# Kernel tuning notes

Measured on AMD Instinct MI355X. Metric: run time of the kernel, lower is better.

## Reference

```python
import jax, jax.numpy as jnp
import numpy as np

IN_CH = 512
OUT_CH = 512
NUM_GROUPS = 32
EPS = 1e-5


def setup_inputs() -> dict:
    key = jax.random.key(0)
    ks = jax.random.split(key, 8)
    N, C, H, W = 4, IN_CH, 64, 64
    s = 0.02
    return {
        "x": jax.random.normal(ks[0], (N, C, H, W), jnp.float32),
        "gn_scale": jnp.ones((C,), jnp.float32),
        "gn_bias": jnp.zeros((C,), jnp.float32),
        "wq": jax.random.normal(ks[1], (OUT_CH, C), jnp.float32) * s,
        "bq": jnp.zeros((OUT_CH,), jnp.float32),
        "wk": jax.random.normal(ks[2], (OUT_CH, C), jnp.float32) * s,
        "bk": jnp.zeros((OUT_CH,), jnp.float32),
        "wv": jax.random.normal(ks[3], (OUT_CH, C), jnp.float32) * s,
        "bv": jnp.zeros((OUT_CH,), jnp.float32),
        "wo": jax.random.normal(ks[4], (OUT_CH, OUT_CH), jnp.float32) * s,
        "bo": jnp.zeros((OUT_CH,), jnp.float32),
    }


def _group_norm(x, scale, bias):
    # x: [N, C, H, W] -> normalize per (group, spatial)
    N, C, H, W = x.shape
    g = x.reshape(N, NUM_GROUPS, C // NUM_GROUPS, H, W)
    mean = jnp.mean(g, axis=(2, 3, 4), keepdims=True)
    var = jnp.var(g, axis=(2, 3, 4), keepdims=True)
    g = (g - mean) * jax.lax.rsqrt(var + EPS)
    h = g.reshape(N, C, H, W)
    return h * scale[None, :, None, None] + bias[None, :, None, None]


def _conv1x1(x, w, b):
    # x: [N, C_in, H, W], w: [C_out, C_in] -> [N, C_out, H, W]
    return jnp.einsum('nchw,dc->ndhw', x, w) + b[None, :, None, None]


def reference(x, gn_scale, gn_bias, wq, bq, wk, bk, wv, bv, wo, bo):
    N, C, H, W = x.shape
    L = H * W
    h = _group_norm(x, gn_scale, gn_bias)
    q = _conv1x1(h, wq, bq).reshape(N, OUT_CH, L)
    k = _conv1x1(h, wk, bk).reshape(N, OUT_CH, L)
    v = _conv1x1(h, wv, bv).reshape(N, OUT_CH, L)
    scores = jnp.einsum('nci,ncj->nij', q, k) * (OUT_CH ** -0.5)  # [N, L, L]
    att = jax.nn.softmax(scores, axis=-1)
    out = jnp.einsum('nij,ncj->nci', att, v).reshape(N, OUT_CH, H, W)
    out = _conv1x1(out, wo, bo)
    return out + x  # skip_proj is Identity since in_ch == out_ch
```

## Files before the change

kernel.cpp:

```cpp
#include <hip/hip_runtime.h>
#include <math.h>

#define NB   4
#define CCH  512
#define LL   4096
#define GRP  32
#define CPG  16
#define CL   (CCH*LL)
#define EPSV 1e-5f
#define QSTR 1024

typedef __bf16 bf16x8 __attribute__((ext_vector_type(8)));
typedef float  f32x4  __attribute__((ext_vector_type(4)));

#define GLOAD_LDS16(g, l) __builtin_amdgcn_global_load_lds( \
    (const __attribute__((address_space(1))) void*)(g),     \
    (__attribute__((address_space(3))) void*)(l), 16, 0, 0)

__device__ __forceinline__ int swz_slot(int row, int q) {
    return 4 * row + (q ^ ((row >> 1) & 3));
}
__device__ __forceinline__ void swz_src(int l, int& jj, int& cc) {
    jj = l >> 2;
    cc = (l & 3) ^ ((l >> 3) & 3);
}

#define DPPF(x, ctrl) __builtin_bit_cast(float, \
    __builtin_amdgcn_update_dpp(0, __builtin_bit_cast(int, (x)), (ctrl), 0xf, 0xf, false))
__device__ __forceinline__ float red_sum16(float x) {
    x += DPPF(x, 0xB1); x += DPPF(x, 0x4E);
    x += DPPF(x, 0x124); x += DPPF(x, 0x128);
    return x;
}

__global__ __launch_bounds__(1024) void gn_stats(const float* __restrict__ x,
                                                 float* __restrict__ stats) {
    int n = blockIdx.x >> 5, g = blockIdx.x & 31;
    size_t base = ((size_t)n * CCH + (size_t)g * CPG) * LL;
    const float4* xp = (const float4*)(x + base);
    const int NV = CPG * LL / 4;
    int tid = threadIdx.x;
    float s1 = 0.f, s2 = 0.f;
    for (int i = tid; i < NV; i += 1024) {
        float4 v = xp[i];
        s1 += v.x + v.y + v.z + v.w;
        s2 += v.x*v.x + v.y*v.y + v.z*v.z + v.w*v.w;
    }
    __shared__ float red[32];
    for (int o = 32; o; o >>= 1) { s1 += __shfl_down(s1, o); s2 += __shfl_down(s2, o); }
    int lane = tid & 63, w = tid >> 6;
    if (!lane) { red[w] = s1; red[16 + w] = s2; }
    __syncthreads();
    if (tid == 0) {
        float a = 0.f, b = 0.f;
        for (int i = 0; i < 16; ++i) { a += red[i]; b += red[16 + i]; }
        const float inv_n = 1.f / (float)(CPG * LL);
        float mean = a * inv_n;
        float var  = b * inv_n - mean * mean;
        stats[blockIdx.x * 2]     = mean;
        stats[blockIdx.x * 2 + 1] = rsqrtf(var + EPSV);
    }
}

__global__ __launch_bounds__(256) void gn_norm_t(const float* __restrict__ x,
    const float* __restrict__ gamma, const float* __restrict__ beta,
    const float* __restrict__ stats, __bf16* __restrict__ Ht) {
    __shared__ float T[64][65];
    int n = blockIdx.z, c0 = blockIdx.y * 64, l0 = blockIdx.x * 64;
    int tid = threadIdx.x;
    int lx = tid & 63, py = tid >> 6;
    const float* xb = x + (size_t)n * CL;
#pragma unroll
    for (int p = 0; p < 16; ++p) {
        int cl = p * 4 + py;
        int c = c0 + cl;
        int g = c >> 4;
        float mean = stats[(n * GRP + g) * 2];
        float rstd = stats[(n * GRP + g) * 2 + 1];
        float sc = gamma[c] * rstd, bi = beta[c] - mean * sc;
        float v = xb[(size_t)c * LL + l0 + lx];
        T[lx][cl] = v * sc + bi;
    }
    __syncthreads();
    __bf16* hb = Ht + (size_t)n * CL;
#pragma unroll
    for (int p = 0; p < 16; ++p) {
        int ll = p * 4 + py;
        hb[(size_t)(l0 + ll) * CCH + c0 + lx] = (__bf16)T[ll][lx];
    }
}

__global__ __launch_bounds__(256) void tobf16_4(
    const float* __restrict__ s0, const float* __restrict__ s1,
    const float* __restrict__ s2, const float* __restrict__ s3,
    __bf16* __restrict__ dst) {
    const float* sp = (blockIdx.y == 0) ? s0 : (blockIdx.y == 1) ? s1
                    : (blockIdx.y == 2) ? s2 : s3;
    int i = (blockIdx.x * 256 + threadIdx.x) * 4;
    float4 v = *(const float4*)(sp + i);
    __bf16* d = dst + (size_t)blockIdx.y * CCH * CCH + i;
    d[0] = (__bf16)v.x; d[1] = (__bf16)v.y; d[2] = (__bf16)v.z; d[3] = (__bf16)v.w;
}

#define BM 128
#define BN 128
#define BK 32

template<int EPI>
__global__ __launch_bounds__(256) void gemm_nt(
    const __bf16* __restrict__ A, const __bf16* __restrict__ B,
    void* __restrict__ Cv, int M, int N, int K,
    long bsA, long bsB, long bsC, long bsR,
    const float* __restrict__ bias, const float* __restrict__ bias2,
    const float* __restrict__ resid)
{
    __shared__ __align__(16) __bf16 As[BM * BK];
    __shared__ __align__(16) __bf16 Bs[BN * BK];
    const int tid = threadIdx.x;
    const int l = tid & 63, w = tid >> 6;
    const int wm = w >> 1, wn = w & 1;
    const int m0 = blockIdx.y * BM, n0 = blockIdx.x * BN;
    A += (long)blockIdx.z * bsA;
    B += (long)blockIdx.z * bsB;

    f32x4 acc[4][4];
#pragma unroll
    for (int i = 0; i < 4; ++i)
#pragma unroll
        for (int j = 0; j < 4; ++j) acc[i][j] = f32x4{0.f, 0.f, 0.f, 0.f};

    int jj, cc; swz_src(l, jj, cc);
    const int slot = swz_slot(l & 15, l >> 4);

    const __bf16* Ag = A + (size_t)(m0 + w * 16 + jj) * K + cc * 8;
    const __bf16* Bg = B + (size_t)(n0 + w * 16 + jj) * K + cc * 8;
    char* AsB = (char*)As + w * 1024;
    char* BsB = (char*)Bs + w * 1024;

    for (int k0 = 0; k0 < K; k0 += BK) {
        GLOAD_LDS16(Ag + k0,                 AsB);
        GLOAD_LDS16(Ag + k0 + (size_t)64*K,  AsB + 4096);
        GLOAD_LDS16(Bg + k0,                 BsB);
        GLOAD_LDS16(Bg + k0 + (size_t)64*K,  BsB + 4096);
        __syncthreads();
        bf16x8 ar[4], br[4];
#pragma unroll
        for (int t = 0; t < 4; ++t) {
            ar[t] = *(const bf16x8*)(As + (wm*64 + t*16) * BK + slot * 8);
            br[t] = *(const bf16x8*)(Bs + (wn*64 + t*16) * BK + slot * 8);
        }
#pragma unroll
        for (int ti = 0; ti < 4; ++ti)
#pragma unroll
            for (int tj = 0; tj < 4; ++tj)
                acc[ti][tj] = __builtin_amdgcn_mfma_f32_16x16x32_bf16(
                    ar[ti], br[tj], acc[ti][tj], 0, 0, 0);
        __syncthreads();
    }

    const long cb = (long)blockIdx.z * bsC;
    const float* bn = (EPI == 5) ? ((n0 < 512) ? bias : (bias2 - 512)) : nullptr;
#pragma unroll
    for (int ti = 0; ti < 4; ++ti) {
#pragma unroll
        for (int r = 0; r < 4; ++r) {
            int m = m0 + wm*64 + ti*16 + (l >> 4)*4 + r;
            float bv = (EPI == 2 || EPI == 4) ? bias[m] : 0.f;
#pragma unroll
            for (int tj = 0; tj < 4; ++tj) {
                int n = n0 + wn*64 + tj*16 + (l & 15);
                float v = acc[ti][tj][r];
                if (EPI == 5) v += bn[n];
                if (EPI == 2 || EPI == 4) v += bv;
                if (EPI == 4) {
                    float rs = resid[(long)blockIdx.z * bsR + (size_t)m * N + n];
                    ((float*)Cv)[cb + (size_t)m * N + n] = v + rs;
                } else {
                    ((__bf16*)Cv)[cb + (size_t)m * N + n] = (__bf16)v;
                }
            }
        }
    }
}

#define PSTR 88

__global__ __launch_bounds__(512, 2) void flash_attn(
    const __bf16* __restrict__ QK, const __bf16* __restrict__ Vb,
    __bf16* __restrict__ Ot)
{
    __shared__ __align__(16) __bf16 Ks[16 * 64 * 32];
    __shared__ __align__(16) __bf16 Vs[2 * 512 * 32];
    __shared__ float  Sm[64 * 68];
    __shared__ __align__(16) __bf16 Ps[64 * PSTR];
    __shared__ float Lp[64 * 2];

    const int tid = threadIdx.x;
    const int l = tid & 63, w = tid >> 6;
    const int wi = w & 1, jh = (w >> 1) & 1, kh = w >> 2;
    const int g = l >> 4, c = l & 15;
    const int b = (blockIdx.x & 7) >> 1;
    const int qt = ((blockIdx.x >> 3) << 1) | (blockIdx.x & 1);
    const int i0 = qt * 64;
    const size_t bb2 = (size_t)b * LL * QSTR;
    const size_t bb  = (size_t)b * CL;
    const float alpha = 0.044194173824159216f;

    int jj, cc; swz_src(l, jj, cc);
    const int slot = swz_slot(c, g);

    bf16x8 Qf[2][8];
    {
        const __bf16* Qg = QK + bb2 + (size_t)(i0 + wi*32 + c) * QSTR + kh*256 + g*8;
#pragma unroll
        for (int mi = 0; mi < 2; ++mi)
#pragma unroll
            for (int kc = 0; kc < 8; ++kc)
                Qf[mi][kc] = *(const bf16x8*)(Qg + (size_t)mi*16*QSTR + kc*32);
    }

    f32x4 Oacc[4][4];
#pragma unroll
    for (int mi = 0; mi < 4; ++mi)
#pragma unroll
        for (int ni = 0; ni < 4; ++ni) Oacc[mi][ni] = f32x4{0.f, 0.f, 0.f, 0.f};
    float l_r[2][4] = {{0.f,0.f,0.f,0.f},{0.f,0.f,0.f,0.f}};

    const __bf16* Kb = QK + bb2 + 512;
    const __bf16* Vg = Vb + bb;

    auto stageK = [&](int j0) {
#pragma unroll
        for (int q = 0; q < 2; ++q) {
            int kc = q * 8 + w;
#pragma unroll
            for (int p = 0; p < 4; ++p) {
                const __bf16* src = Kb + (size_t)(j0 + p*16 + jj) * QSTR + kc*32 + cc*8;
                GLOAD_LDS16(src, (char*)Ks + kc*4096 + p*1024);
            }
        }
    };
    auto stageV = [&](int j0) {
#pragma unroll
        for (int jc = 0; jc < 2; ++jc)
#pragma unroll
            for (int p = 0; p < 4; ++p) {
                const __bf16* src = Vg + (size_t)(w*64 + p*16 + jj) * LL + j0 + jc*32 + cc*8;
                GLOAD_LDS16(src, (char*)Vs + jc*32768 + (w*64 + p*16)*64);
            }
    };

    stageK(0);
    for (int t = 0; t < 64; ++t) {
        __syncthreads();
        stageV(t * 64);

        f32x4 S[2][2];
#pragma unroll
        for (int mi = 0; mi < 2; ++mi)
#pragma unroll
            for (int tj = 0; tj < 2; ++tj) S[mi][tj] = f32x4{0.f,0.f,0.f,0.f};
#pragma unroll
        for (int kc = 0; kc < 8; ++kc) {
#pragma unroll
            for (int tj = 0; tj < 2; ++tj) {
                bf16x8 kf = *(const bf16x8*)(Ks + (kh*8 + kc)*2048 + (jh*2 + tj)*512 + slot*8);
#pragma unroll
                for (int mi = 0; mi < 2; ++mi)
                    S[mi][tj] = __builtin_amdgcn_mfma_f32_16x16x32_bf16(Qf[mi][kc], kf, S[mi][tj], 0, 0, 0);
            }
        }
        if (kh) {
#pragma unroll
            for (int mi = 0; mi < 2; ++mi)
#pragma unroll
                for (int tj = 0; tj < 2; ++tj)
#pragma unroll
                    for (int r = 0; r < 4; ++r)
                        Sm[(wi*32 + mi*16 + g*4 + r)*68 + (jh*2 + tj)*16 + c] = S[mi][tj][r];
        }
        __syncthreads();

        if (!kh) {
#pragma unroll
            for (int mi = 0; mi < 2; ++mi) {
#pragma unroll
                for (int r = 0; r < 4; ++r) {
                    int row = wi*32 + mi*16 + g*4 + r;
                    float rs = 0.f;
#pragma unroll
                    for (int tj = 0; tj < 2; ++tj) {
                        float p = __expf((S[mi][tj][r] + Sm[row*68 + (jh*2 + tj)*16 + c]) * alpha);
                        rs += p;
                        Ps[row * PSTR + (jh*2 + tj)*16 + c] = (__bf16)p;
                    }
                    l_r[mi][r] += rs;
                }
            }
        } else {
            if (t < 63) stageK((t + 1) * 64);
        }
        __syncthreads();
        if (t < 63 && !kh) stageK((t + 1) * 64);

#pragma unroll
        for (int jc = 0; jc < 2; ++jc) {
            bf16x8 pa[4];
#pragma unroll
            for (int mi = 0; mi < 4; ++mi)
                pa[mi] = *(const bf16x8*)(Ps + (mi*16 + c) * PSTR + jc*32 + g*8);
#pragma unroll
            for (int ni = 0; ni < 4; ++ni) {
                bf16x8 vf = *(const bf16x8*)(Vs + jc*16384 + (w*64 + ni*16)*32 + slot*8);
#pragma unroll
                for (int mi = 0; mi < 4; ++mi)
                    Oacc[mi][ni] = __builtin_amdgcn_mfma_f32_16x16x32_bf16(pa[mi], vf, Oacc[mi][ni], 0, 0, 0);
            }
        }
    }

    if (!kh) {
#pragma unroll
        for (int mi = 0; mi < 2; ++mi)
#pragma unroll
            for (int r = 0; r < 4; ++r) {
                float tot = red_sum16(l_r[mi][r]);
                if (c == 0) Lp[(wi*32 + mi*16 + g*4 + r)*2 + jh] = tot;
            }
    }
    __syncthreads();
#pragma unroll
    for (int mi = 0; mi < 4; ++mi) {
#pragma unroll
        for (int r = 0; r < 4; ++r) {
            int row = mi*16 + g*4 + r;
            float inv = 1.f / (Lp[row*2] + Lp[row*2 + 1]);
#pragma unroll
            for (int ni = 0; ni < 4; ++ni) {
                int col = w*64 + ni*16 + c;
                Ot[bb + (size_t)(i0 + row) * CCH + col] = (__bf16)(Oacc[mi][ni][r] * inv);
            }
        }
    }
}

extern "C" void kernel_launch(void* const* d_in, const int* in_sizes, int n_in,
                              void* d_out, int out_size, void* d_ws, size_t ws_size,
                              hipStream_t stream) {
    const float* x   = (const float*)d_in[0];
    const float* gnw = (const float*)d_in[1];
    const float* gnb = (const float*)d_in[2];
    const float* wq  = (const float*)d_in[3];
    const float* bq  = (const float*)d_in[4];
    const float* wk  = (const float*)d_in[5];
    const float* bk  = (const float*)d_in[6];
    const float* wv  = (const float*)d_in[7];
    const float* bv  = (const float*)d_in[8];
    const float* wo  = (const float*)d_in[9];
    const float* bo  = (const float*)d_in[10];
    float* out = (float*)d_out;

    __bf16* wsb = (__bf16*)d_ws;
    const size_t NCL = (size_t)NB * CL;
    __bf16* Ht  = wsb;
    __bf16* QKt = Ht + NCL;
    __bf16* Vb  = QKt + 2 * NCL;
    __bf16* Ot  = Vb + NCL;
    __bf16* Wb  = Ot + NCL;
    float* stats = (float*)(Wb + (size_t)4 * CCH * CCH);
    __bf16* wqkb = Wb;
    __bf16* wvb  = Wb + (size_t)2 * CCH * CCH;
    __bf16* wob  = Wb + (size_t)3 * CCH * CCH;

    tobf16_4<<<dim3(256, 4), 256, 0, stream>>>(wq, wk, wv, wo, Wb);
    gn_stats<<<NB * GRP, 1024, 0, stream>>>(x, stats);
    gn_norm_t<<<dim3(LL / 64, CCH / 64, NB), 256, 0, stream>>>(x, gnw, gnb, stats, Ht);

    gemm_nt<5><<<dim3(1024 / 128, LL / 128, NB), 256, 0, stream>>>(
        Ht, wqkb, QKt, LL, 1024, CCH, CL, 0, (long)LL * 1024, 0, bq, bk, nullptr);
    gemm_nt<2><<<dim3(LL / 128, CCH / 128, NB), 256, 0, stream>>>(
        wvb, Ht, Vb, CCH, LL, CCH, 0, CL, CL, 0, bv, nullptr, nullptr);

    flash_attn<<<dim3(256), 512, 0, stream>>>(QKt, Vb, Ot);

    gemm_nt<4><<<dim3(LL / 128, CCH / 128, NB), 256, 0, stream>>>(
        wob, Ot, (void*)out, CCH, LL, CCH, 0, CL, CL, CL, bo, nullptr, x);
}
```

Before: 388.9 us.

## Double-buffer K tiles, load V directly to registers, split softmax across halves

The flash attention loop now keeps K in two LDS buffers, so the next tile is staged while the current one is consumed, and the extra barrier for K staging is gone. V fragments are read straight from global memory into registers instead of being staged through LDS. The softmax work is split so both kh halves exchange partial scores via a transposed Sm layout and each computes exp for 16 rows, balancing work. The cost is higher register pressure from holding V fragments and uncoalesced direct global V loads.

```diff
diff --git a/kernel.cpp b/kernel.cpp
--- a/kernel.cpp
+++ b/kernel.cpp
@@ -184,14 +184,15 @@
 }
 
 #define PSTR 88
+#define SMSTR 68
 
 __global__ __launch_bounds__(512, 2) void flash_attn(
     const __bf16* __restrict__ QK, const __bf16* __restrict__ Vb,
     __bf16* __restrict__ Ot)
 {
-    __shared__ __align__(16) __bf16 Ks[16 * 64 * 32];
-    __shared__ __align__(16) __bf16 Vs[2 * 512 * 32];
-    __shared__ float  Sm[64 * 68];
+    __shared__ __align__(16) __bf16 Ks0[16 * 64 * 32];
+    __shared__ __align__(16) __bf16 Ks1[16 * 64 * 32];
+    __shared__ __align__(16) float  Sm[64 * SMSTR];
     __shared__ __align__(16) __bf16 Ps[64 * PSTR];
     __shared__ float Lp[64 * 2];
 
@@ -224,109 +225,111 @@
     for (int mi = 0; mi < 4; ++mi)
 #pragma unroll
         for (int ni = 0; ni < 4; ++ni) Oacc[mi][ni] = f32x4{0.f, 0.f, 0.f, 0.f};
-    float l_r[2][4] = {{0.f,0.f,0.f,0.f},{0.f,0.f,0.f,0.f}};
+    float l_r[4] = {0.f, 0.f, 0.f, 0.f};
 
     const __bf16* Kb = QK + bb2 + 512;
     const __bf16* Vg = Vb + bb;
 
-    auto stageK = [&](int j0) {
+    auto stageK = [&](__bf16* dst, int j0) {
 #pragma unroll
         for (int q = 0; q < 2; ++q) {
             int kc = q * 8 + w;
 #pragma unroll
             for (int p = 0; p < 4; ++p) {
                 const __bf16* src = Kb + (size_t)(j0 + p*16 + jj) * QSTR + kc*32 + cc*8;
-                GLOAD_LDS16(src, (char*)Ks + kc*4096 + p*1024);
+                GLOAD_LDS16(src, (char*)dst + kc*4096 + p*1024);
             }
         }
     };
-    auto stageV = [&](int j0) {
-#pragma unroll
-        for (int jc = 0; jc < 2; ++jc)
-#pragma unroll
-            for (int p = 0; p < 4; ++p) {
-                const __bf16* src = Vg + (size_t)(w*64 + p*16 + jj) * LL + j0 + jc*32 + cc*8;
-                GLOAD_LDS16(src, (char*)Vs + jc*32768 + (w*64 + p*16)*64);
-            }
-    };
-
-    stageK(0);
-    for (int t = 0; t < 64; ++t) {
-        __syncthreads();
-        stageV(t * 64);
-
-        f32x4 S[2][2];
-#pragma unroll
-        for (int mi = 0; mi < 2; ++mi)
-#pragma unroll
-            for (int tj = 0; tj < 2; ++tj) S[mi][tj] = f32x4{0.f,0.f,0.f,0.f};
-#pragma unroll
-        for (int kc = 0; kc < 8; ++kc) {
-#pragma unroll
-            for (int tj = 0; tj < 2; ++tj) {
-                bf16x8 kf = *(const bf16x8*)(Ks + (kh*8 + kc)*2048 + (jh*2 + tj)*512 + slot*8);
-#pragma unroll
-                for (int mi = 0; mi < 2; ++mi)
-                    S[mi][tj] = __builtin_amdgcn_mfma_f32_16x16x32_bf16(Qf[mi][kc], kf, S[mi][tj], 0, 0, 0);
-            }
-        }
-        if (kh) {
+
+    stageK(Ks0, 0);
+    __syncthreads();
+
+    for (int tt = 0; tt < 32; ++tt) {
+#pragma unroll
+        for (int h = 0; h < 2; ++h) {
+            const int t = tt * 2 + h;
+            __bf16* const Krd = h ? Ks1 : Ks0;
+            __bf16* const Kst = h ? Ks0 : Ks1;
+
+            bf16x8 vf[2][4];
+            const __bf16* Vt = Vg + t * 64;
+#pragma unroll
+            for (int jc = 0; jc < 2; ++jc)
+#pragma unroll
+                for (int ni = 0; ni < 4; ++ni)
+                    vf[jc][ni] = *(const bf16x8*)(
+                        Vt + (size_t)(w*64 + ni*16 + c) * LL + jc*32 + g*8);
+
+            if (t < 63) stageK(Kst, (t + 1) * 64);
+
+            f32x4 S[2][2];
 #pragma unroll
             for (int mi = 0; mi < 2; ++mi)
 #pragma unroll
+                for (int tj = 0; tj < 2; ++tj) S[mi][tj] = f32x4{0.f,0.f,0.f,0.f};
+#pragma unroll
+            for (int kc = 0; kc < 8; ++kc) {
+#pragma unroll
+                for (int tj = 0; tj < 2; ++tj) {
+                    bf16x8 kf = *(const bf16x8*)(
+                        Krd + (kh*8 + kc)*2048 + (jh*2 + tj)*512 + slot*8);
+#pragma unroll
+                    for (int mi = 0; mi < 2; ++mi)
+                        S[mi][tj] = __builtin_amdgcn_mfma_f32_16x16x32_bf16(
+                            Qf[mi][kc], kf, S[mi][tj], 0, 0, 0);
+                }
+            }
+            {
+                const int me = 1 - kh;
+#pragma unroll
                 for (int tj = 0; tj < 2; ++tj)
-#pragma unroll
-                    for (int r = 0; r < 4; ++r)
-                        Sm[(wi*32 + mi*16 + g*4 + r)*68 + (jh*2 + tj)*16 + c] = S[mi][tj][r];
-        }
-        __syncthreads();
-
-        if (!kh) {
-#pragma unroll
-            for (int mi = 0; mi < 2; ++mi) {
+                    *(f32x4*)&Sm[(jh*32 + tj*16 + c) * SMSTR + wi*32 + me*16 + g*4]
+                        = S[me][tj];
+            }
+            __syncthreads();
+
+            {
+                f32x4 part[2];
+#pragma unroll
+                for (int tj = 0; tj < 2; ++tj)
+                    part[tj] = *(const f32x4*)&Sm[(jh*32 + tj*16 + c) * SMSTR
+                                                  + wi*32 + kh*16 + g*4];
+                const int row0 = wi*32 + kh*16 + g*4;
 #pragma unroll
                 for (int r = 0; r < 4; ++r) {
-                    int row = wi*32 + mi*16 + g*4 + r;
                     float rs = 0.f;
 #pragma unroll
                     for (int tj = 0; tj < 2; ++tj) {
-                        float p = __expf((S[mi][tj][r] + Sm[row*68 + (jh*2 + tj)*16 + c]) * alpha);
+                        float p = __expf((S[kh][tj][r] + part[tj][r]) * alpha);
                         rs += p;
-                        Ps[row * PSTR + (jh*2 + tj)*16 + c] = (__bf16)p;
+                        Ps[(row0 + r) * PSTR + jh*32 + tj*16 + c] = (__bf16)p;
                     }
-                    l_r[mi][r] += rs;
+                    l_r[r] += rs;
                 }
             }
-        } else {
-            if (t < 63) stageK((t + 1) * 64);
-        }
-        __syncthreads();
-        if (t < 63 && !kh) stageK((t + 1) * 64);
-
-#pragma unroll
-        for (int jc = 0; jc < 2; ++jc) {
-            bf16x8 pa[4];
-#pragma unroll
-            for (int mi = 0; mi < 4; ++mi)
-                pa[mi] = *(const bf16x8*)(Ps + (mi*16 + c) * PSTR + jc*32 + g*8);
-#pragma unroll
-            for (int ni = 0; ni < 4; ++ni) {
-                bf16x8 vf = *(const bf16x8*)(Vs + jc*16384 + (w*64 + ni*16)*32 + slot*8);
+            __syncthreads();
+
+#pragma unroll
+            for (int jc = 0; jc < 2; ++jc) {
+                bf16x8 pa[4];
 #pragma unroll
                 for (int mi = 0; mi < 4; ++mi)
-                    Oacc[mi][ni] = __builtin_amdgcn_mfma_f32_16x16x32_bf16(pa[mi], vf, Oacc[mi][ni], 0, 0, 0);
-            }
-        }
-    }
-
-    if (!kh) {
-#pragma unroll
-        for (int mi = 0; mi < 2; ++mi)
-#pragma unroll
-            for (int r = 0; r < 4; ++r) {
-                float tot = red_sum16(l_r[mi][r]);
-                if (c == 0) Lp[(wi*32 + mi*16 + g*4 + r)*2 + jh] = tot;
-            }
+                    pa[mi] = *(const bf16x8*)(Ps + (mi*16 + c) * PSTR + jc*32 + g*8);
+#pragma unroll
+                for (int ni = 0; ni < 4; ++ni)
+#pragma unroll
+                    for (int mi = 0; mi < 4; ++mi)
+                        Oacc[mi][ni] = __builtin_amdgcn_mfma_f32_16x16x32_bf16(
+                            pa[mi], vf[jc][ni], Oacc[mi][ni], 0, 0, 0);
+            }
+        }
+    }
+
+#pragma unroll
+    for (int r = 0; r < 4; ++r) {
+        float tot = red_sum16(l_r[r]);
+        if (c == 0) Lp[(wi*32 + kh*16 + g*4 + r)*2 + jh] = tot;
     }
     __syncthreads();
 #pragma unroll
```

Result: slower. 525.3 us (+35.1%).

## Split softmax exp work across both K-half waves and add MFMA priority hints

Applied to the files above, without the earlier changes.

Before, the waves owning the second K half only wrote partial scores, and the first-half waves did all the exp and P writes. Now each wave sends the partial for the other half's rows and computes exp for its own 16 rows, so softmax work is split evenly and K staging no longer alternates by role. s_setprio calls also raise wave priority around the MFMA loops. The row-sum bookkeeping becomes per-wave, and the final Lp reduction gathers from both kh groups. This trades a symmetric partial-sum exchange through Sm for better load balance.

```diff
diff --git a/kernel.cpp b/kernel.cpp
--- a/kernel.cpp
+++ b/kernel.cpp
@@ -224,7 +224,7 @@
     for (int mi = 0; mi < 4; ++mi)
 #pragma unroll
         for (int ni = 0; ni < 4; ++ni) Oacc[mi][ni] = f32x4{0.f, 0.f, 0.f, 0.f};
-    float l_r[2][4] = {{0.f,0.f,0.f,0.f},{0.f,0.f,0.f,0.f}};
+    float l_r[4] = {0.f, 0.f, 0.f, 0.f};
 
     const __bf16* Kb = QK + bb2 + 512;
     const __bf16* Vg = Vb + bb;
@@ -250,6 +250,29 @@
             }
     };
 
+    auto expst = [&](const f32x4 (&Sx)[2]) {
+        const int er0 = wi*32 + (1 - kh)*16 + g*4;
+#pragma unroll
+        for (int tj = 0; tj < 2; ++tj)
+#pragma unroll
+            for (int r = 0; r < 4; ++r)
+                Sm[(er0 + r)*68 + (jh*2 + tj)*16 + c] = Sx[tj][r];
+    };
+    auto smx = [&](const f32x4 (&Sown)[2]) {
+        const int row0 = wi*32 + kh*16 + g*4;
+#pragma unroll
+        for (int r = 0; r < 4; ++r) {
+            float rs = 0.f;
+#pragma unroll
+            for (int tj = 0; tj < 2; ++tj) {
+                float p = __expf((Sown[tj][r] + Sm[(row0 + r)*68 + (jh*2 + tj)*16 + c]) * alpha);
+                rs += p;
+                Ps[(row0 + r) * PSTR + (jh*2 + tj)*16 + c] = (__bf16)p;
+            }
+            l_r[r] += rs;
+        }
+    };
+
     stageK(0);
     for (int t = 0; t < 64; ++t) {
         __syncthreads();
@@ -260,6 +283,7 @@
         for (int mi = 0; mi < 2; ++mi)
 #pragma unroll
             for (int tj = 0; tj < 2; ++tj) S[mi][tj] = f32x4{0.f,0.f,0.f,0.f};
+        __builtin_amdgcn_s_setprio(1);
 #pragma unroll
         for (int kc = 0; kc < 8; ++kc) {
 #pragma unroll
@@ -270,39 +294,16 @@
                     S[mi][tj] = __builtin_amdgcn_mfma_f32_16x16x32_bf16(Qf[mi][kc], kf, S[mi][tj], 0, 0, 0);
             }
         }
-        if (kh) {
-#pragma unroll
-            for (int mi = 0; mi < 2; ++mi)
-#pragma unroll
-                for (int tj = 0; tj < 2; ++tj)
-#pragma unroll
-                    for (int r = 0; r < 4; ++r)
-                        Sm[(wi*32 + mi*16 + g*4 + r)*68 + (jh*2 + tj)*16 + c] = S[mi][tj][r];
-        }
-        __syncthreads();
-
-        if (!kh) {
-#pragma unroll
-            for (int mi = 0; mi < 2; ++mi) {
-#pragma unroll
-                for (int r = 0; r < 4; ++r) {
-                    int row = wi*32 + mi*16 + g*4 + r;
-                    float rs = 0.f;
-#pragma unroll
-                    for (int tj = 0; tj < 2; ++tj) {
-                        float p = __expf((S[mi][tj][r] + Sm[row*68 + (jh*2 + tj)*16 + c]) * alpha);
-                        rs += p;
-                        Ps[row * PSTR + (jh*2 + tj)*16 + c] = (__bf16)p;
-                    }
-                    l_r[mi][r] += rs;
-                }
-            }
-        } else {
-            if (t < 63) stageK((t + 1) * 64);
-        }
-        __syncthreads();
-        if (t < 63 && !kh) stageK((t + 1) * 64);
-
+        __builtin_amdgcn_s_setprio(0);
+
+        if (kh) expst(S[0]); else expst(S[1]);
+        __syncthreads();
+
+        if (kh) smx(S[1]); else smx(S[0]);
+        __syncthreads();
+        if (t < 63) stageK((t + 1) * 64);
+
+        __builtin_amdgcn_s_setprio(1);
 #pragma unroll
         for (int jc = 0; jc < 2; ++jc) {
             bf16x8 pa[4];
@@ -317,16 +318,13 @@
                     Oacc[mi][ni] = __builtin_amdgcn_mfma_f32_16x16x32_bf16(pa[mi], vf, Oacc[mi][ni], 0, 0, 0);
             }
         }
-    }
-
-    if (!kh) {
-#pragma unroll
-        for (int mi = 0; mi < 2; ++mi)
-#pragma unroll
-            for (int r = 0; r < 4; ++r) {
-                float tot = red_sum16(l_r[mi][r]);
-                if (c == 0) Lp[(wi*32 + mi*16 + g*4 + r)*2 + jh] = tot;
-            }
+        __builtin_amdgcn_s_setprio(0);
+    }
+
+#pragma unroll
+    for (int r = 0; r < 4; ++r) {
+        float tot = red_sum16(l_r[r]);
+        if (c == 0) Lp[(wi*32 + kh*16 + g*4 + r)*2 + jh] = tot;
     }
     __syncthreads();
 #pragma unroll
```

Result: faster. 367.9 us (-5.4%).
